# Kernel optimization log

Hardware: AMD Instinct MI355X
Metric: run time of the kernel (lower is better)

## Reference

```python
import jax, jax.numpy as jnp
import numpy as np

B_, L, D_MODEL = 2, 4096, 2048
H, P, N, G, K = 32, 64, 128, 1, 4
EPS = 1e-5
INTER = H * P                      # 2048
CONV_DIM = INTER + 2 * G * N       # 2304
PROJ = INTER + CONV_DIM + H        # 4384


def setup_inputs() -> dict:
    key = jax.random.key(0)
    ks = jax.random.split(key, 5)
    hidden_states = jax.random.normal(ks[0], (B_, L, D_MODEL), jnp.float32)
    W_in = jax.random.normal(ks[1], (PROJ, D_MODEL), jnp.float32) * 0.02
    conv_w = jax.random.normal(ks[2], (CONV_DIM, K), jnp.float32) * 0.1
    conv_b = jnp.zeros((CONV_DIM,), jnp.float32)
    dt_bias = jnp.ones((H,), jnp.float32)
    A_log = jnp.log(jnp.arange(1, H + 1, dtype=jnp.float32))
    D_param = jnp.ones((H,), jnp.float32)
    norm_w = jnp.ones((INTER,), jnp.float32)
    W_out = jax.random.normal(ks[3], (D_MODEL, INTER), jnp.float32) * 0.02
    return dict(hidden_states=hidden_states, W_in=W_in, conv_w=conv_w, conv_b=conv_b,
                dt_bias=dt_bias, A_log=A_log, D_param=D_param, norm_w=norm_w, W_out=W_out)


def _silu(x):
    return x * jax.nn.sigmoid(x)


def _mamba2_mixer(hidden_states, W_in, conv_w, conv_b, dt_bias, A_log, D_param, norm_w, W_out):
    b, l, _ = hidden_states.shape
    # in_proj (no bias): [b, l, PROJ]
    proj = jnp.einsum('bld,pd->blp', hidden_states, W_in)
    gate = proj[..., :INTER]                     # [b, l, INTER]
    hBC = proj[..., INTER:INTER + CONV_DIM]      # [b, l, CONV_DIM]
    dt = proj[..., INTER + CONV_DIM:]            # [b, l, H]

    # depthwise causal conv1d + silu
    xc = jnp.transpose(hBC, (0, 2, 1))           # [b, C, l]
    conv = jax.lax.conv_general_dilated(
        xc, conv_w[:, None, :], window_strides=(1,), padding=[(K - 1, 0)],
        dimension_numbers=('NCH', 'OIH', 'NCH'), feature_group_count=CONV_DIM)
    hBC = _silu(jnp.transpose(conv + conv_b[None, :, None], (0, 2, 1)))  # [b, l, CONV_DIM]

    xs = hBC[..., :INTER].reshape(b, l, H, P)                 # [b, l, H, P]
    Bm = hBC[..., INTER:INTER + G * N].reshape(b, l, G, N)    # [b, l, G, N]
    Cm = hBC[..., INTER + G * N:].reshape(b, l, G, N)
    Bh = jnp.repeat(Bm, H // G, axis=2)                       # [b, l, H, N]
    Ch = jnp.repeat(Cm, H // G, axis=2)

    # dt softplus with bias; A = -exp(A_log)
    dt = jax.nn.softplus(dt + dt_bias)                        # [b, l, H]
    A = -jnp.exp(A_log)                                       # [H]
    dA = jnp.exp(dt * A)                                      # [b, l, H]

    # sequential selective scan over time (state h: [b, H, P, N])
    def step(h, inp):
        dA_t, dt_t, x_t, B_t, C_t = inp
        u = (dt_t[:, :, None] * x_t)[..., None] * B_t[:, :, None, :]   # [b,H,P,N]
        h = dA_t[:, :, None, None] * h + u
        y = jnp.einsum('bhpn,bhn->bhp', h, C_t)
        return h, y

    tm = lambda a: jnp.moveaxis(a, 1, 0)  # time-major
    h0 = jnp.zeros((b, H, P, N), hidden_states.dtype)
    _, ys = jax.lax.scan(step, h0, (tm(dA), tm(dt), tm(xs), tm(Bh), tm(Ch)))
    y = jnp.moveaxis(ys, 0, 1) + D_param[None, None, :, None] * xs   # [b, l, H, P]
    y = y.reshape(b, l, INTER)

    # gated RMSNorm (norm_before_gate=False, single group)
    g = y * _silu(gate)
    g = g * jax.lax.rsqrt(jnp.mean(g * g, axis=-1, keepdims=True) + EPS) * norm_w

    return jnp.einsum('bli,di->bld', g, W_out)   # [b, l, D_MODEL]


def reference(hidden_states, W_in, conv_w, conv_b, dt_bias, A_log, D_param, norm_w, W_out):
    return _mamba2_mixer(hidden_states, W_in, conv_w, conv_b, dt_bias, A_log, D_param, norm_w, W_out)
```

## Files before the change

kernel.cpp:

```cpp
#include <hip/hip_runtime.h>
#include <cstdint>
#include <cstddef>

#define B_        2
#define LSEQ      4096
#define DMODEL    2048
#define NH        32
#define PDIM      64
#define NSTATE    128
#define KCONV     4
#define INTER     2048
#define CONV_DIM  2304
#define HBCDT     2336
#define HBCDT_PAD 2432
#define WH_ROWS   2560
#define ROWS      (B_*LSEQ)
#define NC        32
#define CLEN      (LSEQ/NC)

typedef unsigned short ushort_t;
typedef short bf16x8 __attribute__((ext_vector_type(8)));
typedef float f32x4 __attribute__((ext_vector_type(4)));

__device__ __forceinline__ float siluf(float x) {
  return x / (1.0f + __expf(-x));
}
__device__ __forceinline__ float bf2f(ushort_t u) {
  union { unsigned int i; float f; } v; v.i = ((unsigned int)u) << 16; return v.f;
}
__device__ __forceinline__ ushort_t f2bf(float f) {
  union { float f; unsigned int i; } v; v.f = f;
  unsigned int r = v.i + 0x7fff + ((v.i >> 16) & 1);
  return (ushort_t)(r >> 16);
}
__device__ __forceinline__ void async16(const void* g, void* l) {
  __builtin_amdgcn_global_load_lds(
      (const __attribute__((address_space(1))) unsigned int*)g,
      (__attribute__((address_space(3))) unsigned int*)l, 16, 0, 0);
}

__global__ __launch_bounds__(256) void cvt_f32_bf16(
    const float* __restrict__ src, ushort_t* __restrict__ dst, int n) {
  const int i = (blockIdx.x * 256 + threadIdx.x) * 4;
  if (i >= n) return;
  float4 v = *(const float4*)(src + i);
  ushort4 o; o.x = f2bf(v.x); o.y = f2bf(v.y); o.z = f2bf(v.z); o.w = f2bf(v.w);
  *(ushort4*)(dst + i) = o;
}

__global__ __launch_bounds__(256) void cvt_Wh(
    const float* __restrict__ W_in, ushort_t* __restrict__ dst) {
  const int i = (blockIdx.x * 256 + threadIdx.x) * 4;
  if (i >= WH_ROWS * DMODEL) return;
  const int r = i / DMODEL, c = i % DMODEL;
  ushort4 o;
  if (r < HBCDT) {
    float4 v = *(const float4*)(W_in + (size_t)(INTER + r) * DMODEL + c);
    o.x = f2bf(v.x); o.y = f2bf(v.y); o.z = f2bf(v.z); o.w = f2bf(v.w);
  } else {
    o.x = 0; o.y = 0; o.z = 0; o.w = 0;
  }
  *(ushort4*)(dst + i) = o;
}

#define STAGE_A(CN, H, KTT) do {                                              \
    async16(Ast + (size_t)((H) * 128) * 2048 + (KTT) * 64,                    \
            smem_ + (CN) + (H) * 16384 + wave * 1024);                        \
    async16(Ast + (size_t)((H) * 128 + 64) * 2048 + (KTT) * 64,               \
            smem_ + (CN) + (H) * 16384 + 8192 + wave * 1024);                 \
  } while (0)

#define STAGE_B(CN, H, KTT) do {                                              \
    async16(Bst + (size_t)((H) * 128) * 2048 + (KTT) * 64,                    \
            smem_ + 65536 + (CN) + (H) * 16384 + wave * 1024);                \
    async16(Bst + (size_t)((H) * 128 + 64) * 2048 + (KTT) * 64,               \
            smem_ + 65536 + (CN) + (H) * 16384 + 8192 + wave * 1024);         \
  } while (0)

#define LDA(DST, CB, MH) do {                                                 \
    const char* ab_ = smem_ + (CB) + aro;                                     \
    _Pragma("unroll") for (int mi_ = 0; mi_ < 4; ++mi_) {                     \
      DST[mi_][0] = *(const bf16x8*)(ab_ + (MH) * 8192 + mi_ * 2048 + g0);    \
      DST[mi_][1] = *(const bf16x8*)(ab_ + (MH) * 8192 + mi_ * 2048 + g1);    \
    }                                                                         \
  } while (0)

#define LDB(DST, CB, NHH) do {                                                \
    const char* bb_ = smem_ + 65536 + (CB) + bro;                             \
    _Pragma("unroll") for (int ni_ = 0; ni_ < 2; ++ni_) {                     \
      DST[ni_][0] = *(const bf16x8*)(bb_ + (NHH) * 4096 + ni_ * 2048 + g0);   \
      DST[ni_][1] = *(const bf16x8*)(bb_ + (NHH) * 4096 + ni_ * 2048 + g1);   \
    }                                                                         \
  } while (0)

#define MFMAQ(MH, NHH, AF, BF)                                                \
  _Pragma("unroll") for (int mi_ = 0; mi_ < 4; ++mi_)                         \
  _Pragma("unroll") for (int ni_ = 0; ni_ < 2; ++ni_) {                       \
    f32x4& c_ = acc[(MH) * 4 + mi_][(NHH) * 2 + ni_];                         \
    c_ = __builtin_amdgcn_mfma_f32_16x16x32_bf16(AF[mi_][0], BF[ni_][0], c_, 0, 0, 0); \
    c_ = __builtin_amdgcn_mfma_f32_16x16x32_bf16(AF[mi_][1], BF[ni_][1], c_, 0, 0, 0); \
  }

#define PH(X) do {                                                            \
    __builtin_amdgcn_s_barrier();                                             \
    __builtin_amdgcn_s_setprio(1);                                            \
    X;                                                                        \
    __builtin_amdgcn_s_setprio(0);                                            \
    __builtin_amdgcn_s_barrier();                                             \
  } while (0)

#define GROUP_TAIL_CNT(X, DOSTAGE, CN, KTT) do {                              \
    __builtin_amdgcn_s_barrier();                                             \
    __builtin_amdgcn_s_setprio(1);                                            \
    X;                                                                        \
    __builtin_amdgcn_s_setprio(0);                                            \
    if (DOSTAGE) {                                                            \
      STAGE_A(CN, 0, KTT); STAGE_A(CN, 1, KTT);                               \
      STAGE_B(CN, 0, KTT); STAGE_B(CN, 1, KTT);                               \
      asm volatile("s_waitcnt vmcnt(8)" ::: "memory");                        \
    } else {                                                                  \
      asm volatile("s_waitcnt vmcnt(0)" ::: "memory");                        \
    }                                                                         \
    __builtin_amdgcn_s_barrier();                                             \
  } while (0)

template <bool OUT_BF16, int NTN, int NVALID, int LDC>
__global__ __launch_bounds__(512, 2) void gemm256_nt(
    const ushort_t* __restrict__ A, const ushort_t* __restrict__ B,
    void* __restrict__ C) {
  __shared__ __align__(16) char smem_[131072];
  const int t    = threadIdx.x;
  const int lane = t & 63;
  const int wave = t >> 6;
  const int wm   = wave >> 2;
  const int wn   = wave & 3;

  constexpr int NWG = NTN * 32;
  int bid = blockIdx.y * NTN + blockIdx.x;
  bid = (bid & 7) * (NWG >> 3) + (bid >> 3);
  const int m0 = (bid / NTN) * 256;
  const int n0 = (bid % NTN) * 256;

  const int srow = wave * 8 + (lane >> 3);
  const int scol = ((lane & 7) ^ (lane >> 3)) * 8;
  const ushort_t* Ast = A + (size_t)(m0 + srow) * 2048 + scol;
  const ushort_t* Bst = B + (size_t)(n0 + srow) * 2048 + scol;

  const int aro = (wm * 128 + (lane & 15)) * 128;
  const int bro = (wn * 64 + (lane & 15)) * 128;
  const int g0  = ((lane >> 4) ^ (lane & 7)) * 16;
  const int g1  = (((lane >> 4) + 4) ^ (lane & 7)) * 16;

  f32x4 acc[8][4];
#pragma unroll
  for (int i = 0; i < 8; ++i)
#pragma unroll
    for (int j = 0; j < 4; ++j) {
      f32x4 z = {0.f, 0.f, 0.f, 0.f};
      acc[i][j] = z;
    }
  bf16x8 af[4][2], bq0[2][2], bq1[2][2];

  STAGE_A(0, 0, 0); STAGE_A(0, 1, 0);
  STAGE_B(0, 0, 0); STAGE_B(0, 1, 0);
  STAGE_A(32768, 0, 1); STAGE_A(32768, 1, 1);
  STAGE_B(32768, 0, 1); STAGE_B(32768, 1, 1);
  asm volatile("s_waitcnt vmcnt(8)" ::: "memory");
  __builtin_amdgcn_s_barrier();

  constexpr int NT = 2048 / 64;
  for (int kt = 0; kt < NT; kt += 2) {
    LDA(af, 0, 0); LDB(bq0, 0, 0);
    PH(MFMAQ(0, 0, af, bq0));
    LDB(bq1, 0, 1);
    PH(MFMAQ(0, 1, af, bq1));
    LDA(af, 0, 1);
    PH(MFMAQ(1, 0, af, bq0));
    GROUP_TAIL_CNT(MFMAQ(1, 1, af, bq1), (kt + 2) < NT, 0, kt + 2);
    LDA(af, 32768, 0); LDB(bq0, 32768, 0);
    PH(MFMAQ(0, 0, af, bq0));
    LDB(bq1, 32768, 1);
    PH(MFMAQ(0, 1, af, bq1));
    LDA(af, 32768, 1);
    PH(MFMAQ(1, 0, af, bq0));
    GROUP_TAIL_CNT(MFMAQ(1, 1, af, bq1), (kt + 3) < NT, 32768, kt + 3);
  }

  const int mb = m0 + wm * 128 + (lane >> 4) * 4;
  const int nb = n0 + wn * 64 + (lane & 15);
#pragma unroll
  for (int mq = 0; mq < 8; ++mq)
#pragma unroll
    for (int nq = 0; nq < 4; ++nq)
#pragma unroll
      for (int r = 0; r < 4; ++r) {
        const int m = mb + mq * 16 + r;
        const int n = nb + nq * 16;
        if (n < NVALID) {
          if (OUT_BF16)
            ((ushort_t*)C)[(size_t)m * LDC + n] = f2bf(acc[mq][nq][r]);
          else
            ((float*)C)[(size_t)m * LDC + n] = acc[mq][nq][r];
        }
      }
}

__global__ __launch_bounds__(256) void conv_silu_kernel(
    const ushort_t* __restrict__ hbcdt, const float* __restrict__ conv_w,
    const float* __restrict__ conv_b, ushort_t* __restrict__ convo,
    ushort_t* __restrict__ BT_g) {
  const int idx = blockIdx.x * 256 + threadIdx.x;
  if (idx >= ROWS * CONV_DIM) return;
  const int c   = idx % CONV_DIM;
  const int row = idx / CONV_DIM;
  const int l   = row & (LSEQ - 1);
  float acc = conv_b[c];
  const float* w = conv_w + c * KCONV;
#pragma unroll
  for (int k = 0; k < KCONV; ++k) {
    const int tt = l + k - (KCONV - 1);
    if (tt >= 0)
      acc = fmaf(bf2f(hbcdt[(size_t)(row + k - (KCONV - 1)) * HBCDT_PAD + c]), w[k], acc);
  }
  const ushort_t v = f2bf(siluf(acc));
  convo[idx] = v;
  if (c >= INTER && c < INTER + NSTATE) {
    const int n   = c - INTER;
    const int bb  = row >> 12;
    const int cch = l >> 7;
    const int sl  = l & (CLEN - 1);
    BT_g[(((size_t)bb * NC + cch) * NSTATE + n) * CLEN + sl] = v;
  }
}

__global__ __launch_bounds__(256) void dtprep_kernel(
    const ushort_t* __restrict__ hbcdt, const float* __restrict__ dt_bias,
    float* __restrict__ dt_s) {
  const int idx = blockIdx.x * 256 + threadIdx.x;
  if (idx >= ROWS * NH) return;
  const int h   = idx & (NH - 1);
  const int row = idx >> 5;
  float x = bf2f(hbcdt[(size_t)row * HBCDT_PAD + CONV_DIM + h]) + dt_bias[h];
  dt_s[idx] = (x > 20.f) ? x : log1pf(__expf(x));
}

#define XLD 272
__global__ __launch_bounds__(256) void scan_state_kernel(
    const ushort_t* __restrict__ convo, const float* __restrict__ dt_s,
    const float* __restrict__ A_log, const ushort_t* __restrict__ BT_g,
    ushort_t* __restrict__ Sbuf, float* __restrict__ chunkA) {
  __shared__ __align__(16) char XwT[64 * XLD];
  __shared__ float dt_sh[CLEN];
  __shared__ float wgt[CLEN];

  const int blk = blockIdx.x;
  const int c   = blk & (NC - 1);
  const int h   = (blk >> 5) & 31;
  const int b   = blk >> 10;
  const int t   = threadIdx.x;
  const int lane = t & 63;
  const int wave = t >> 6;
  const size_t crow = (size_t)(b * LSEQ + c * CLEN);

  if (t < CLEN) dt_sh[t] = dt_s[(crow + t) * NH + h];
  __syncthreads();

  if (wave == 0) {
    const float a = __expf(A_log[h]);
    float v0 = -a * dt_sh[lane];
    float v1 = -a * dt_sh[lane + 64];
#pragma unroll
    for (int off = 1; off < 64; off <<= 1) {
      float u0 = __shfl_up(v0, off);
      float u1 = __shfl_up(v1, off);
      if (lane >= off) { v0 += u0; v1 += u1; }
    }
    const float tot0 = __shfl(v0, 63);
    const float La0  = v0;
    const float La1  = v1 + tot0;
    const float Lend = __shfl(v1, 63) + tot0;
    wgt[lane]      = dt_sh[lane]      * __expf(Lend - La0);
    wgt[lane + 64] = dt_sh[lane + 64] * __expf(Lend - La1);
    if (lane == 0) chunkA[(b * NH + h) * NC + c] = __expf(Lend);
  }
  __syncthreads();

  {
    const int p = lane;
    const int xcol = h * PDIM + p;
#pragma unroll
    for (int oct = 0; oct < 4; ++oct) {
      const int t0 = wave * 32 + oct * 8;
      unsigned int pk[4];
#pragma unroll
      for (int e = 0; e < 4; ++e) {
        const float f0 = bf2f(convo[(crow + t0 + 2*e)     * CONV_DIM + xcol]) * wgt[t0 + 2*e];
        const float f1 = bf2f(convo[(crow + t0 + 2*e + 1) * CONV_DIM + xcol]) * wgt[t0 + 2*e + 1];
        pk[e] = (unsigned int)f2bf(f0) | ((unsigned int)f2bf(f1) << 16);
      }
      *(uint4*)(XwT + p * XLD + t0 * 2) = make_uint4(pk[0], pk[1], pk[2], pk[3]);
    }
  }
  __syncthreads();

  f32x4 acc[8];
#pragma unroll
  for (int j = 0; j < 8; ++j) {
    f32x4 z = {0.f, 0.f, 0.f, 0.f};
    acc[j] = z;
  }
  const int rowA = wave * 16 + (lane & 15);
  const int koff = (lane >> 4) * 8;
  const ushort_t* Bt = BT_g + ((size_t)b * NC + c) * NSTATE * CLEN;
#pragma unroll
  for (int k0 = 0; k0 < 4; ++k0) {
    bf16x8 af = *(const bf16x8*)(XwT + rowA * XLD + (k0 * 32 + koff) * 2);
#pragma unroll
    for (int j = 0; j < 8; ++j) {
      bf16x8 bfx = *(const bf16x8*)(Bt + (size_t)(j * 16 + (lane & 15)) * CLEN + k0 * 32 + koff);
      acc[j] = __builtin_amdgcn_mfma_f32_16x16x32_bf16(af, bfx, acc[j], 0, 0, 0);
    }
  }

  ushort_t* Sb = Sbuf + (((size_t)b * NC + c) * NH + h) * (PDIM * NSTATE);
  const int prow = wave * 16 + (lane >> 4) * 4;
  const int ncol = lane & 15;
#pragma unroll
  for (int j = 0; j < 8; ++j)
#pragma unroll
    for (int r = 0; r < 4; ++r)
      Sb[(size_t)(prow + r) * NSTATE + j * 16 + ncol] = f2bf(acc[j][r]);
}

__global__ __launch_bounds__(256) void state_combine_kernel(
    ushort_t* __restrict__ Sbuf, const float* __restrict__ chunkA) {
  const int idx = blockIdx.x * 256 + threadIdx.x;
  const int nq = idx & 31;
  const int p  = (idx >> 5) & 63;
  const int h  = (idx >> 11) & 31;
  const int b  = (idx >> 16) & 1;
  const float* ca = chunkA + (b * NH + h) * NC;

  float s0 = 0.f, s1 = 0.f, s2 = 0.f, s3 = 0.f;
#pragma unroll 4
  for (int c = 0; c < NC; ++c) {
    const size_t off = ((((size_t)b * NC + c) * NH + h) * PDIM + p) * NSTATE + nq * 4;
    ushort4 loc = *(const ushort4*)(Sbuf + off);
    ushort4 o;
    o.x = f2bf(s0); o.y = f2bf(s1); o.z = f2bf(s2); o.w = f2bf(s3);
    *(ushort4*)(Sbuf + off) = o;
    const float a = ca[c];
    s0 = fmaf(a, s0, bf2f(loc.x));
    s1 = fmaf(a, s1, bf2f(loc.y));
    s2 = fmaf(a, s2, bf2f(loc.z));
    s3 = fmaf(a, s3, bf2f(loc.w));
  }
}

#define WLD 272
__global__ __launch_bounds__(256) void ssd_y_kernel(
    const ushort_t* __restrict__ convo, const float* __restrict__ dt_s,
    const float* __restrict__ A_log, const float* __restrict__ D_param,
    const ushort_t* __restrict__ Sbuf, ushort_t* __restrict__ ybuf) {
  __shared__ __align__(16) char XT[64 * 256];
  __shared__ __align__(16) char Wsh[128 * WLD];
  __shared__ float dt_sh[CLEN];
  __shared__ float La[CLEN];

  const int blk = blockIdx.x;
  const int c   = blk & (NC - 1);
  const int h   = (blk >> 5) & 31;
  const int b   = blk >> 10;
  const int t   = threadIdx.x;
  const int lane = t & 63;
  const int wave = t >> 6;

  const size_t crow = (size_t)(b * LSEQ + c * CLEN);

  {
    const int p = lane;
    const int xcol = h * PDIM + p;
#pragma unroll
    for (int oct = 0; oct < 4; ++oct) {
      const int tl0 = wave * 32 + oct * 8;
      unsigned int pk[4];
#pragma unroll
      for (int e = 0; e < 4; ++e) {
        ushort_t v0 = convo[(crow + tl0 + 2 * e) * CONV_DIM + xcol];
        ushort_t v1 = convo[(crow + tl0 + 2 * e + 1) * CONV_DIM + xcol];
        pk[e] = (unsigned int)v0 | ((unsigned int)v1 << 16);
      }
      const int tsw = tl0 ^ ((p & 7) << 3);
      *(uint4*)(XT + p * 256 + tsw * 2) = make_uint4(pk[0], pk[1], pk[2], pk[3]);
    }
  }
  if (t < CLEN) dt_sh[t] = dt_s[(crow + t) * NH + h];
  __syncthreads();

  if (wave == 0) {
    const float a = __expf(A_log[h]);
    float v0 = -a * dt_sh[lane];
    float v1 = -a * dt_sh[lane + 64];
#pragma unroll
    for (int off = 1; off < 64; off <<= 1) {
      float u0 = __shfl_up(v0, off);
      float u1 = __shfl_up(v1, off);
      if (lane >= off) { v0 += u0; v1 += u1; }
    }
    const float tot0 = __shfl(v0, 63);
    La[lane]      = v0;
    La[lane + 64] = v1 + tot0;
  }
  __syncthreads();

  const int wt = wave & 1;
  const int ws = wave >> 1;
  const bool active = !(wt == 0 && ws == 1);

  f32x4 g[4][4];
#pragma unroll
  for (int i = 0; i < 4; ++i)
#pragma unroll
    for (int j = 0; j < 4; ++j) {
      f32x4 z = {0.f, 0.f, 0.f, 0.f};
      g[i][j] = z;
    }

  if (active) {
    for (int k0 = 0; k0 < 4; ++k0) {
      const int koct = k0 * 32 + (lane >> 4) * 8;
      bf16x8 cf[4], bfg[4];
#pragma unroll
      for (int i = 0; i < 4; ++i) {
        const int tg = wt * 64 + i * 16 + (lane & 15);
        cf[i] = *(const bf16x8*)(convo + (crow + tg) * CONV_DIM + INTER + NSTATE + koct);
        const int sg = ws * 64 + i * 16 + (lane & 15);
        bfg[i] = *(const bf16x8*)(convo + (crow + sg) * CONV_DIM + INTER + koct);
      }
#pragma unroll
      for (int i = 0; i < 4; ++i)
#pragma unroll
        for (int j = 0; j < 4; ++j)
          g[i][j] = __builtin_amdgcn_mfma_f32_16x16x32_bf16(cf[i], bfg[j], g[i][j], 0, 0, 0);
    }
  }
#pragma unroll
  for (int i = 0; i < 4; ++i) {
    const int tbase = wt * 64 + i * 16 + ((lane >> 4) << 2);
    float Lat[4];
#pragma unroll
    for (int r = 0; r < 4; ++r) Lat[r] = La[tbase + r];
#pragma unroll
    for (int j = 0; j < 4; ++j) {
      const int sl  = ws * 64 + j * 16 + (lane & 15);
      const float Las = La[sl];
      const float dts = dt_sh[sl];
#pragma unroll
      for (int r = 0; r < 4; ++r) {
        const int tl = tbase + r;
        float val = 0.f;
        if (active && tl >= sl)
          val = g[i][j][r] * dts * __expf(Lat[r] - Las);
        *(ushort_t*)(Wsh + tl * WLD + sl * 2) = f2bf(val);
      }
    }
  }
  __syncthreads();

  const int yt = wave & 1;
  const int yp = wave >> 1;
  f32x4 acc[4][2];
#pragma unroll
  for (int i = 0; i < 4; ++i)
#pragma unroll
    for (int j = 0; j < 2; ++j) {
      f32x4 z = {0.f, 0.f, 0.f, 0.f};
      acc[i][j] = z;
    }

  const ushort_t* Sb = Sbuf + (((size_t)b * NC + c) * NH + h) * PDIM * NSTATE;

  for (int k0 = 0; k0 < 4; ++k0) {
    const int koct = k0 * 32 + (lane >> 4) * 8;
    bf16x8 af[4], sf[2];
#pragma unroll
    for (int i = 0; i < 4; ++i) {
      const int tg = yt * 64 + i * 16 + (lane & 15);
      af[i] = *(const bf16x8*)(convo + (crow + tg) * CONV_DIM + INTER + NSTATE + koct);
    }
#pragma unroll
    for (int j = 0; j < 2; ++j) {
      const int pr = yp * 32 + j * 16 + (lane & 15);
      sf[j] = *(const bf16x8*)(Sb + pr * NSTATE + koct);
    }
#pragma unroll
    for (int i = 0; i < 4; ++i)
#pragma unroll
      for (int j = 0; j < 2; ++j)
        acc[i][j] = __builtin_amdgcn_mfma_f32_16x16x32_bf16(af[i], sf[j], acc[i][j], 0, 0, 0);
  }
#pragma unroll
  for (int i = 0; i < 4; ++i) {
    const int tbase = yt * 64 + i * 16 + ((lane >> 4) << 2);
#pragma unroll
    for (int r = 0; r < 4; ++r) {
      const float e = __expf(La[tbase + r]);
#pragma unroll
      for (int j = 0; j < 2; ++j) acc[i][j][r] *= e;
    }
  }
  for (int k0 = 0; k0 < 4; ++k0) {
    const int koct = k0 * 32 + (lane >> 4) * 8;
    bf16x8 wf[4], xf[2];
#pragma unroll
    for (int i = 0; i < 4; ++i) {
      const int tl = yt * 64 + i * 16 + (lane & 15);
      wf[i] = *(const bf16x8*)(Wsh + tl * WLD + koct * 2);
    }
#pragma unroll
    for (int j = 0; j < 2; ++j) {
      const int pr  = yp * 32 + j * 16 + (lane & 15);
      const int tsw = koct ^ ((pr & 7) << 3);
      xf[j] = *(const bf16x8*)(XT + pr * 256 + tsw * 2);
    }
#pragma unroll
    for (int i = 0; i < 4; ++i)
#pragma unroll
      for (int j = 0; j < 2; ++j)
        acc[i][j] = __builtin_amdgcn_mfma_f32_16x16x32_bf16(wf[i], xf[j], acc[i][j], 0, 0, 0);
  }

  const float Dh = D_param[h];
#pragma unroll
  for (int i = 0; i < 4; ++i) {
    const int tbase = yt * 64 + i * 16 + ((lane >> 4) << 2);
#pragma unroll
    for (int j = 0; j < 2; ++j) {
      const int pr = yp * 32 + j * 16 + (lane & 15);
#pragma unroll
      for (int r = 0; r < 4; ++r) {
        const int tl  = tbase + r;
        const int tsw = tl ^ ((pr & 7) << 3);
        const float x = bf2f(*(const ushort_t*)(XT + pr * 256 + tsw * 2));
        ybuf[(crow + tl) * INTER + h * PDIM + pr] = f2bf(acc[i][j][r] + Dh * x);
      }
    }
  }
}

__global__ __launch_bounds__(256) void gated_rmsnorm_kernel(
    ushort_t* __restrict__ y, const ushort_t* __restrict__ gate,
    const float* __restrict__ norm_w) {
  const int row = blockIdx.x;
  ushort_t* yr = y + (size_t)row * INTER;
  const ushort_t* gr = gate + (size_t)row * INTER;
  const int t  = threadIdx.x;
  const int i0 = t * 8;

  ushort4 ya = *(const ushort4*)(yr + i0);
  ushort4 yb = *(const ushort4*)(yr + i0 + 4);
  ushort4 ga = *(const ushort4*)(gr + i0);
  ushort4 gb = *(const ushort4*)(gr + i0 + 4);

  float g[8];
  g[0] = bf2f(ya.x) * siluf(bf2f(ga.x));
  g[1] = bf2f(ya.y) * siluf(bf2f(ga.y));
  g[2] = bf2f(ya.z) * siluf(bf2f(ga.z));
  g[3] = bf2f(ya.w) * siluf(bf2f(ga.w));
  g[4] = bf2f(yb.x) * siluf(bf2f(gb.x));
  g[5] = bf2f(yb.y) * siluf(bf2f(gb.y));
  g[6] = bf2f(yb.z) * siluf(bf2f(gb.z));
  g[7] = bf2f(yb.w) * siluf(bf2f(gb.w));

  float ss = 0.f;
#pragma unroll
  for (int i = 0; i < 8; ++i) ss += g[i] * g[i];

  ss += __shfl_xor(ss, 32);
  ss += __shfl_xor(ss, 16);
  ss += __shfl_xor(ss, 8);
  ss += __shfl_xor(ss, 4);
  ss += __shfl_xor(ss, 2);
  ss += __shfl_xor(ss, 1);

  __shared__ float red[4];
  if ((t & 63) == 0) red[t >> 6] = ss;
  __syncthreads();
  const float tot = red[0] + red[1] + red[2] + red[3];
  const float scale = rsqrtf(tot * (1.0f / INTER) + 1e-5f);

  ushort4 o0, o1;
  o0.x = f2bf(g[0] * scale * norm_w[i0 + 0]);
  o0.y = f2bf(g[1] * scale * norm_w[i0 + 1]);
  o0.z = f2bf(g[2] * scale * norm_w[i0 + 2]);
  o0.w = f2bf(g[3] * scale * norm_w[i0 + 3]);
  o1.x = f2bf(g[4] * scale * norm_w[i0 + 4]);
  o1.y = f2bf(g[5] * scale * norm_w[i0 + 5]);
  o1.z = f2bf(g[6] * scale * norm_w[i0 + 6]);
  o1.w = f2bf(g[7] * scale * norm_w[i0 + 7]);
  *(ushort4*)(yr + i0)     = o0;
  *(ushort4*)(yr + i0 + 4) = o1;
}

extern "C" void kernel_launch(void* const* d_in, const int* in_sizes, int n_in,
                              void* d_out, int out_size, void* d_ws, size_t ws_size,
                              hipStream_t stream) {
  const float* hs      = (const float*)d_in[0];
  const float* W_in    = (const float*)d_in[1];
  const float* conv_w  = (const float*)d_in[2];
  const float* conv_b  = (const float*)d_in[3];
  const float* dt_bias = (const float*)d_in[4];
  const float* A_log   = (const float*)d_in[5];
  const float* D_param = (const float*)d_in[6];
  const float* norm_w  = (const float*)d_in[7];
  const float* W_out   = (const float*)d_in[8];
  float* out = (float*)d_out;

  char* ws = (char*)d_ws;
  size_t off = 0;
  ushort_t* hbcdt_bf = (ushort_t*)(ws + off); off += (size_t)ROWS * HBCDT_PAD * 2;
  ushort_t* convo    = (ushort_t*)(ws + off); off += (size_t)ROWS * CONV_DIM * 2;
  float*    dt_s     = (float*)(ws + off);    off += (size_t)ROWS * NH * 4;
  ushort_t* Wh_bf    = (ushort_t*)(ws + off); off += (size_t)WH_ROWS * DMODEL * 2;
  ushort_t* Wg_bf    = (ushort_t*)(ws + off); off += (size_t)DMODEL * DMODEL * 2;
  ushort_t* Wout_bf  = (ushort_t*)(ws + off); off += (size_t)DMODEL * DMODEL * 2;
  float*    chunkA   = (float*)(ws + off);    off += (size_t)B_ * NH * NC * 4;
  ushort_t* BT_g     = (ushort_t*)(ws + off); off += (size_t)B_ * NC * NSTATE * CLEN * 2;
  ushort_t* ybuf_bf  = hbcdt_bf;

  char* outc = (char*)d_out;
  ushort_t* gate_bf = (ushort_t*)outc;
  ushort_t* hs_bf   = (ushort_t*)(outc + (size_t)ROWS * INTER * 2);
  ushort_t* Sbuf    = hs_bf;

  cvt_f32_bf16<<<(ROWS * DMODEL / 4 + 255) / 256, 256, 0, stream>>>(
      hs, hs_bf, ROWS * DMODEL);
  cvt_Wh<<<(WH_ROWS * DMODEL / 4 + 255) / 256, 256, 0, stream>>>(W_in, Wh_bf);
  cvt_f32_bf16<<<(DMODEL * DMODEL / 4 + 255) / 256, 256, 0, stream>>>(
      W_in, Wg_bf, DMODEL * DMODEL);
  cvt_f32_bf16<<<(DMODEL * DMODEL / 4 + 255) / 256, 256, 0, stream>>>(
      W_out, Wout_bf, DMODEL * DMODEL);

  gemm256_nt<true, 10, HBCDT_PAD, HBCDT_PAD><<<dim3(10, 32), 512, 0, stream>>>(
      hs_bf, Wh_bf, hbcdt_bf);
  gemm256_nt<true, 8, INTER, INTER><<<dim3(8, 32), 512, 0, stream>>>(
      hs_bf, Wg_bf, gate_bf);
  conv_silu_kernel<<<(ROWS * CONV_DIM + 255) / 256, 256, 0, stream>>>(
      hbcdt_bf, conv_w, conv_b, convo, BT_g);
  dtprep_kernel<<<(ROWS * NH + 255) / 256, 256, 0, stream>>>(
      hbcdt_bf, dt_bias, dt_s);
  scan_state_kernel<<<B_ * NH * NC, 256, 0, stream>>>(
      convo, dt_s, A_log, BT_g, Sbuf, chunkA);
  state_combine_kernel<<<(B_ * NH * PDIM * (NSTATE / 4)) / 256, 256, 0, stream>>>(
      Sbuf, chunkA);
  ssd_y_kernel<<<B_ * NH * NC, 256, 0, stream>>>(
      convo, dt_s, A_log, D_param, Sbuf, ybuf_bf);
  gated_rmsnorm_kernel<<<ROWS, 256, 0, stream>>>(ybuf_bf, gate_bf, norm_w);
  gemm256_nt<false, 8, DMODEL, DMODEL><<<dim3(8, 32), 512, 0, stream>>>(
      ybuf_bf, Wout_bf, out);
}
```

Measured before the change: 632.8 us.

## Use 256x320 tile GEMM for the hBC/dt input projection

Adds a specialized GEMM kernel with 256x320 output tiles (each wave computes 128x80) for the hBC+dt part of the input projection. The grid drops from 10x32 to 8x32 workgroups, so 2560 padded rows are covered in fewer tiles, which should balance better against the 256 compute units and reduce redundant A-tile loads. The larger tile needs more LDS (about 144KB), which limits occupancy and may change pipelining behaviour.

After: 594.6 us. 1.06x faster.

```diff
diff --git a/kernel.cpp b/kernel.cpp
--- a/kernel.cpp
+++ b/kernel.cpp
@@ -205,6 +205,132 @@
       }
 }
 
+#define ST_A64(CN, HB, KTT)                                                   \
+    async16(Ast + (size_t)((HB) * 64) * 2048 + (KTT) * 64,                    \
+            smem_ + (CN) + (HB) * 8192 + wave * 1024)
+#define ST_B64(CN, HB, KTT)                                                   \
+    async16(Bst + (size_t)((HB) * 64) * 2048 + (KTT) * 64,                    \
+            smem_ + 65536 + (CN) + (HB) * 8192 + wave * 1024)
+#define STAGE9(ACN, BCN, KTT) do {                                            \
+    ST_A64(ACN, 0, KTT); ST_A64(ACN, 1, KTT);                                 \
+    ST_A64(ACN, 2, KTT); ST_A64(ACN, 3, KTT);                                 \
+    ST_B64(BCN, 0, KTT); ST_B64(BCN, 1, KTT); ST_B64(BCN, 2, KTT);            \
+    ST_B64(BCN, 3, KTT); ST_B64(BCN, 4, KTT);                                 \
+  } while (0)
+
+#define LDB3(DST, BCN) do {                                                   \
+    const char* bb_ = smem_ + 65536 + (BCN) + bro;                            \
+    _Pragma("unroll") for (int ni_ = 0; ni_ < 3; ++ni_) {                     \
+      DST[ni_][0] = *(const bf16x8*)(bb_ + ni_ * 2048 + g0);                  \
+      DST[ni_][1] = *(const bf16x8*)(bb_ + ni_ * 2048 + g1);                  \
+    }                                                                         \
+  } while (0)
+
+#define LDB2(DST, BCN) do {                                                   \
+    const char* bb_ = smem_ + 65536 + (BCN) + bro;                            \
+    _Pragma("unroll") for (int ni_ = 0; ni_ < 2; ++ni_) {                     \
+      DST[ni_][0] = *(const bf16x8*)(bb_ + (3 + ni_) * 2048 + g0);            \
+      DST[ni_][1] = *(const bf16x8*)(bb_ + (3 + ni_) * 2048 + g1);            \
+    }                                                                         \
+  } while (0)
+
+#define MFMA_G(MH, NB, NCNT, AF, BF)                                          \
+  _Pragma("unroll") for (int mi_ = 0; mi_ < 4; ++mi_)                         \
+  _Pragma("unroll") for (int ni_ = 0; ni_ < NCNT; ++ni_) {                    \
+    f32x4& c_ = acc[(MH) * 4 + mi_][(NB) + ni_];                              \
+    c_ = __builtin_amdgcn_mfma_f32_16x16x32_bf16(AF[mi_][0], BF[ni_][0], c_, 0, 0, 0); \
+    c_ = __builtin_amdgcn_mfma_f32_16x16x32_bf16(AF[mi_][1], BF[ni_][1], c_, 0, 0, 0); \
+  }
+
+#define GROUP_TAIL9(X, DOSTAGE, ACN, BCN, KTT) do {                           \
+    __builtin_amdgcn_s_barrier();                                             \
+    __builtin_amdgcn_s_setprio(1);                                            \
+    X;                                                                        \
+    __builtin_amdgcn_s_setprio(0);                                            \
+    if (DOSTAGE) {                                                            \
+      STAGE9(ACN, BCN, KTT);                                                  \
+      asm volatile("s_waitcnt vmcnt(9)" ::: "memory");                        \
+    } else {                                                                  \
+      asm volatile("s_waitcnt vmcnt(0)" ::: "memory");                        \
+    }                                                                         \
+    __builtin_amdgcn_s_barrier();                                             \
+  } while (0)
+
+template <int NTN, int NVALID, int LDC>
+__global__ __launch_bounds__(512, 2) void gemm320_nt(
+    const ushort_t* __restrict__ A, const ushort_t* __restrict__ B,
+    ushort_t* __restrict__ C) {
+  __shared__ __align__(16) char smem_[147456];
+  const int t    = threadIdx.x;
+  const int lane = t & 63;
+  const int wave = t >> 6;
+  const int wm   = wave >> 2;
+  const int wn   = wave & 3;
+
+  constexpr int NWG = NTN * 32;
+  int bid = blockIdx.y * NTN + blockIdx.x;
+  bid = (bid & 7) * (NWG >> 3) + (bid >> 3);
+  const int m0 = (bid / NTN) * 256;
+  const int n0 = (bid % NTN) * 320;
+
+  const int srow = wave * 8 + (lane >> 3);
+  const int scol = ((lane & 7) ^ (lane >> 3)) * 8;
+  const ushort_t* Ast = A + (size_t)(m0 + srow) * 2048 + scol;
+  const ushort_t* Bst = B + (size_t)(n0 + srow) * 2048 + scol;
+
+  const int aro = (wm * 128 + (lane & 15)) * 128;
+  const int bro = (wn * 80 + (lane & 15)) * 128;
+  const int g0  = ((lane >> 4) ^ (lane & 7)) * 16;
+  const int g1  = (((lane >> 4) + 4) ^ (lane & 7)) * 16;
+
+  f32x4 acc[8][5];
+#pragma unroll
+  for (int i = 0; i < 8; ++i)
+#pragma unroll
+    for (int j = 0; j < 5; ++j) {
+      f32x4 z = {0.f, 0.f, 0.f, 0.f};
+      acc[i][j] = z;
+    }
+  bf16x8 af[4][2], bqA[3][2], bqB[2][2];
+
+  STAGE9(0, 0, 0);
+  STAGE9(32768, 40960, 1);
+  asm volatile("s_waitcnt vmcnt(9)" ::: "memory");
+  __builtin_amdgcn_s_barrier();
+
+  constexpr int NT = 2048 / 64;
+  for (int kt = 0; kt < NT; kt += 2) {
+    LDA(af, 0, 0); LDB3(bqA, 0);
+    PH(MFMA_G(0, 0, 3, af, bqA));
+    LDB2(bqB, 0);
+    PH(MFMA_G(0, 3, 2, af, bqB));
+    LDA(af, 0, 1);
+    PH(MFMA_G(1, 0, 3, af, bqA));
+    GROUP_TAIL9(MFMA_G(1, 3, 2, af, bqB), (kt + 2) < NT, 0, 0, kt + 2);
+    LDA(af, 32768, 0); LDB3(bqA, 40960);
+    PH(MFMA_G(0, 0, 3, af, bqA));
+    LDB2(bqB, 40960);
+    PH(MFMA_G(0, 3, 2, af, bqB));
+    LDA(af, 32768, 1);
+    PH(MFMA_G(1, 0, 3, af, bqA));
+    GROUP_TAIL9(MFMA_G(1, 3, 2, af, bqB), (kt + 3) < NT, 32768, 40960, kt + 3);
+  }
+
+  const int mb = m0 + wm * 128 + (lane >> 4) * 4;
+  const int nb = n0 + wn * 80 + (lane & 15);
+#pragma unroll
+  for (int mq = 0; mq < 8; ++mq)
+#pragma unroll
+    for (int nq = 0; nq < 5; ++nq)
+#pragma unroll
+      for (int r = 0; r < 4; ++r) {
+        const int m = mb + mq * 16 + r;
+        const int n = nb + nq * 16;
+        if (n < NVALID)
+          C[(size_t)m * LDC + n] = f2bf(acc[mq][nq][r]);
+      }
+}
+
 __global__ __launch_bounds__(256) void conv_silu_kernel(
     const ushort_t* __restrict__ hbcdt, const float* __restrict__ conv_w,
     const float* __restrict__ conv_b, ushort_t* __restrict__ convo,
@@ -641,7 +767,7 @@
   cvt_f32_bf16<<<(DMODEL * DMODEL / 4 + 255) / 256, 256, 0, stream>>>(
       W_out, Wout_bf, DMODEL * DMODEL);
 
-  gemm256_nt<true, 10, HBCDT_PAD, HBCDT_PAD><<<dim3(10, 32), 512, 0, stream>>>(
+  gemm320_nt<8, HBCDT_PAD, HBCDT_PAD><<<dim3(8, 32), 512, 0, stream>>>(
       hs_bf, Wh_bf, hbcdt_bf);
   gemm256_nt<true, 8, INTER, INTER><<<dim3(8, 32), 512, 0, stream>>>(
       hs_bf, Wg_bf, gate_bf);
```
